# Kernel tuning notes

Measured on AMD Instinct MI355X. Metric: run time of the kernel, lower is better.

The kernel has to match this reference:

```python
import jax, jax.numpy as jnp
import numpy as np

CAPACITY_FACTOR = 1.0  # fairseq Top1Gate default


def setup_inputs() -> dict:
    key = jax.random.key(0)
    ks = jax.random.split(key, 5)
    B, T, M, H, O, E = 8, 1024, 1024, 4096, 1024, 4
    return {
        "hidden_states": jax.random.normal(ks[0], (B, T, M), jnp.float32),
        "gate_w": jax.random.normal(ks[1], (M, E), jnp.float32) * 0.02,
        "fc1_w": jax.random.normal(ks[2], (E, M, H), jnp.float32) * 0.02,
        "fc1_b": jnp.zeros((E, H), jnp.float32),
        "fc2_w": jax.random.normal(ks[3], (E, H, O), jnp.float32) * 0.02,
        "fc2_b": jnp.zeros((E, O), jnp.float32),
    }


def reference(hidden_states, gate_w, fc1_w, fc1_b, fc2_w, fc2_b):
    B, T, M = hidden_states.shape
    E = gate_w.shape[1]
    S = B * T
    C = int(CAPACITY_FACTOR * -(-S // E))  # ceil(S/E)

    features = hidden_states.reshape(S, M)  # [S, M]

    # ---- Top1 gate (fairseq top1gating, eval path: no shuffle/noise) ----
    logits = features @ gate_w                      # [S, E]
    gates = jax.nn.softmax(logits, axis=1)          # [S, E]
    idx = jnp.argmax(gates, axis=1)                 # [S]
    mask1 = jax.nn.one_hot(idx, E, dtype=gates.dtype)  # [S, E]

    # load-balancing aux loss (computed before capacity dropping)
    me = jnp.mean(gates, axis=0)
    ce = jnp.mean(mask1, axis=0)
    l_aux = jnp.sum(me * ce) * E

    # capacity: position within each expert's queue; drop overflow tokens
    locations = jnp.cumsum(mask1, axis=0) - 1.0     # [S, E]
    mask1 = mask1 * (locations < C)
    loc_s = jnp.sum(locations * mask1, axis=1).astype(jnp.int32)  # [S]
    gates1_s = jnp.sum(gates * mask1, axis=1)       # [S] gate value (0 if dropped)

    # combine_weights [S, E, C] and boolean dispatch mask (as float for mm)
    combine = (gates1_s[:, None, None] * mask1[:, :, None]
               * jax.nn.one_hot(loc_s, C, dtype=gates.dtype)[:, None, :])
    dispatch = (combine > 0).astype(features.dtype)  # [S, E, C]

    # ---- dispatch via dense one-hot matmul: [E*C, S] @ [S, M] ----
    dispatch_ecs = jnp.transpose(dispatch, (1, 2, 0)).reshape(E * C, S)
    dispatched = (dispatch_ecs @ features).reshape(E, C, M)

    # ---- per-expert MLP (grouped GEMM) ----
    h = jax.nn.gelu(jnp.einsum('ecm,emh->ech', dispatched, fc1_w) + fc1_b[:, None, :])
    expert_out = jnp.einsum('ech,eho->eco', h, fc2_w) + fc2_b[:, None, :]  # [E, C, O]

    # ---- combine via dense matmul: [S, E*C] @ [E*C, O] ----
    O = expert_out.shape[-1]
    combined = combine.reshape(S, E * C) @ expert_out.reshape(E * C, O)

    return combined.reshape(B, T, O), l_aux
```

## Files before the change

kernel.cpp:

```cpp
#include <hip/hip_runtime.h>
#include <stdint.h>

#define S_TOK 8192
#define MDIM  1024
#define HDIM  4096
#define ODIM  1024
#define NEXP  4
#define CAP   2048

typedef __attribute__((ext_vector_type(8))) short short8;
typedef __attribute__((ext_vector_type(4))) float floatx4;

__device__ __forceinline__ unsigned short f2bf(float x) {
  union { float f; unsigned u; } v; v.f = x;
  unsigned r = v.u + 0x7FFFu + ((v.u >> 16) & 1u);
  return (unsigned short)(r >> 16);
}

__device__ __forceinline__ void gl_lds16(const void* g, void* l) {
  __builtin_amdgcn_global_load_lds(
      (const __attribute__((address_space(1))) void*)g,
      (__attribute__((address_space(3))) void*)l, 16, 0, 0);
}

__device__ __forceinline__ float gelu_tanh(float x) {
  float z = 0.7978845608028654f * (x + 0.044715f * x * x * x);
  float t = 1.0f - 2.0f / (__expf(2.0f * z) + 1.0f);
  return 0.5f * x * (1.0f + t);
}

__global__ __launch_bounds__(256) void gate_kernel(
    const float* __restrict__ feat, const float* __restrict__ gw,
    int* __restrict__ idx, float* __restrict__ gval, float* __restrict__ gsum)
{
  int wave = threadIdx.x >> 6, lane = threadIdx.x & 63;
  int s = blockIdx.x * 4 + wave;
  const float* f = feat + (size_t)s * MDIM;
  double a0 = 0, a1 = 0, a2 = 0, a3 = 0;
  #pragma unroll
  for (int j = 0; j < 16; ++j) {
    int m = lane + j * 64;
    float x = f[m];
    float4 w = ((const float4*)gw)[m];
    a0 += (double)x * w.x; a1 += (double)x * w.y;
    a2 += (double)x * w.z; a3 += (double)x * w.w;
  }
  #pragma unroll
  for (int off = 32; off; off >>= 1) {
    a0 += __shfl_down(a0, off); a1 += __shfl_down(a1, off);
    a2 += __shfl_down(a2, off); a3 += __shfl_down(a3, off);
  }
  __shared__ float bs[4];
  if (threadIdx.x < 4) bs[threadIdx.x] = 0.f;
  __syncthreads();
  if (lane == 0) {
    double lg[4] = {a0, a1, a2, a3};
    double mx = lg[0]; int bi = 0;
    #pragma unroll
    for (int e = 1; e < 4; ++e) if (lg[e] > mx) { mx = lg[e]; bi = e; }
    float ex[4]; float den = 0.f;
    #pragma unroll
    for (int e = 0; e < 4; ++e) { ex[e] = __expf((float)(lg[e] - mx)); den += ex[e]; }
    float inv = 1.f / den;
    idx[s]  = bi;
    gval[s] = ex[bi] * inv;
    #pragma unroll
    for (int e = 0; e < 4; ++e) atomicAdd(&bs[e], ex[e] * inv);
  }
  __syncthreads();
  if (threadIdx.x < 4) atomicAdd(&gsum[threadIdx.x], bs[threadIdx.x]);
}

__global__ __launch_bounds__(1024) void scan_kernel(
    const int* __restrict__ idx, int* __restrict__ perm,
    int* __restrict__ ne, const float* __restrict__ gsum,
    float* __restrict__ laux)
{
  const int tid = threadIdx.x, wave = tid >> 6, lane = tid & 63;
  __shared__ int cnt[16][4];
  __shared__ int off[16][4];
  __shared__ int tot[4];
  unsigned long long below = (lane == 0) ? 0ull : ((~0ull) >> (64 - lane));

  int myE[8], loc[8];
  int c[4] = {0, 0, 0, 0};
  #pragma unroll
  for (int j = 0; j < 8; ++j) {
    int s = wave * 512 + j * 64 + lane;
    int ev = idx[s];
    myE[j] = ev;
    #pragma unroll
    for (int e = 0; e < 4; ++e) {
      unsigned long long mb = __ballot(ev == e);
      if (ev == e) loc[j] = c[e] + __popcll(mb & below);
      c[e] += __popcll(mb);
    }
  }
  if (lane == 0) {
    #pragma unroll
    for (int e = 0; e < 4; ++e) cnt[wave][e] = c[e];
  }
  __syncthreads();
  if (tid < 64) {
    int w = tid >> 2, e = tid & 3;
    int o = 0;
    for (int w2 = 0; w2 < 16; ++w2) if (w2 < w) o += cnt[w2][e];
    off[w][e] = o;
    if (w == 15) tot[e] = o + cnt[15][e];
  }
  __syncthreads();
  #pragma unroll
  for (int j = 0; j < 8; ++j) {
    int s = wave * 512 + j * 64 + lane;
    int e = myE[j];
    int rank = off[wave][e] + loc[j];
    if (rank < CAP) perm[e * CAP + rank] = s;
  }
  if (tid < 4) ne[tid] = tot[tid] < CAP ? tot[tid] : CAP;
  if (tid == 0) {
    float l = 0.f;
    #pragma unroll
    for (int e = 0; e < 4; ++e)
      l += (gsum[e] * (1.0f / S_TOK)) * ((float)tot[e] * (1.0f / S_TOK));
    *laux = l * (float)NEXP;
  }
}

__global__ __launch_bounds__(256) void transpose_cast(
    const float* __restrict__ in, unsigned short* __restrict__ out, int R, int Cc)
{
  __shared__ unsigned short tile[64][66];
  in  += (size_t)blockIdx.z * R * Cc;
  out += (size_t)blockIdx.z * R * Cc;
  int c0 = blockIdx.x * 64, r0 = blockIdx.y * 64;
  int tx = threadIdx.x & 15;
  int ty = threadIdx.x >> 4;
  #pragma unroll
  for (int p = 0; p < 4; ++p) {
    int r = ty + p * 16;
    float4 v = *(const float4*)(in + (size_t)(r0 + r) * Cc + c0 + tx * 4);
    tile[r][tx * 4 + 0] = f2bf(v.x);
    tile[r][tx * 4 + 1] = f2bf(v.y);
    tile[r][tx * 4 + 2] = f2bf(v.z);
    tile[r][tx * 4 + 3] = f2bf(v.w);
  }
  __syncthreads();
  #pragma unroll
  for (int p = 0; p < 4; ++p) {
    int c = ty + p * 16;
    ushort4 o;
    o.x = tile[tx * 4 + 0][c];
    o.y = tile[tx * 4 + 1][c];
    o.z = tile[tx * 4 + 2][c];
    o.w = tile[tx * 4 + 3][c];
    *(ushort4*)(out + (size_t)(c0 + c) * R + r0 + tx * 4) = o;
  }
}

__global__ __launch_bounds__(256) void gather_kernel(
    const float* __restrict__ feat, const int* __restrict__ perm,
    const int* __restrict__ ne, unsigned short* __restrict__ disp)
{
  int b = blockIdx.x;
  int e = b >> 11, c = b & (CAP - 1);
  int m = threadIdx.x * 4;
  ushort4 o;
  if (c < ne[e]) {
    int s = perm[b];
    float4 v = *(const float4*)(feat + (size_t)s * MDIM + m);
    o.x = f2bf(v.x); o.y = f2bf(v.y); o.z = f2bf(v.z); o.w = f2bf(v.w);
  } else {
    o.x = o.y = o.z = o.w = 0;
  }
  *(ushort4*)(disp + (size_t)b * MDIM + m) = o;
}

__global__ __launch_bounds__(256) void fc1_kernel(
    const unsigned short* __restrict__ A, const unsigned short* __restrict__ Bt,
    const float* __restrict__ b1, unsigned short* __restrict__ Hb)
{
  const int e = blockIdx.z, nb = blockIdx.x, mb = blockIdx.y;
  const int tid = threadIdx.x, wave = tid >> 6, lane = tid & 63;

  __shared__ __align__(16) unsigned short smA[128 * 32];
  __shared__ __align__(16) unsigned short smB[128 * 32];

  const char* Ag = (const char*)(A + ((size_t)e * CAP + (size_t)mb * 128) * MDIM);
  const char* Bg = (const char*)(Bt + ((size_t)e * HDIM + (size_t)nb * 128) * MDIM);

  int boff0 = (wave * 2 + 0) * 1024 + lane * 16;
  int boff1 = (wave * 2 + 1) * 1024 + lane * 16;
  const char* agp0 = Ag + (size_t)(boff0 >> 6) * 2048 + (boff0 & 63);
  const char* agp1 = Ag + (size_t)(boff1 >> 6) * 2048 + (boff1 & 63);
  const char* bgp0 = Bg + (size_t)(boff0 >> 6) * 2048 + (boff0 & 63);
  const char* bgp1 = Bg + (size_t)(boff1 >> 6) * 2048 + (boff1 & 63);
  unsigned short* sA0 = smA + (wave * 2 + 0) * 512;
  unsigned short* sA1 = smA + (wave * 2 + 1) * 512;
  unsigned short* sB0 = smB + (wave * 2 + 0) * 512;
  unsigned short* sB1 = smB + (wave * 2 + 1) * 512;

  const int wm = (wave & 1) * 64, wn = (wave >> 1) * 64;
  const int fr = lane & 15, fq = lane >> 4;

  floatx4 acc[4][4] = {};

  for (int kt = 0; kt < MDIM / 32; ++kt) {
    int kb = kt * 64;
    gl_lds16(agp0 + kb, sA0);
    gl_lds16(agp1 + kb, sA1);
    gl_lds16(bgp0 + kb, sB0);
    gl_lds16(bgp1 + kb, sB1);
    __syncthreads();
    short8 af[4], bfr[4];
    #pragma unroll
    for (int i = 0; i < 4; ++i)
      af[i] = *(const short8*)&smA[(wm + i * 16 + fr) * 32 + fq * 8];
    #pragma unroll
    for (int j = 0; j < 4; ++j)
      bfr[j] = *(const short8*)&smB[(wn + j * 16 + fr) * 32 + fq * 8];
    #pragma unroll
    for (int i = 0; i < 4; ++i)
      #pragma unroll
      for (int j = 0; j < 4; ++j)
        acc[i][j] = __builtin_amdgcn_mfma_f32_16x16x32_bf16(af[i], bfr[j], acc[i][j], 0, 0, 0);
    __syncthreads();
  }

  unsigned short* Hrow = Hb + (size_t)e * CAP * HDIM;
  #pragma unroll
  for (int j = 0; j < 4; ++j) {
    int gn = nb * 128 + wn + j * 16 + fr;
    float bv = b1[e * HDIM + gn];
    #pragma unroll
    for (int i = 0; i < 4; ++i) {
      int m0 = mb * 128 + wm + i * 16 + fq * 4;
      #pragma unroll
      for (int r = 0; r < 4; ++r)
        Hrow[(size_t)(m0 + r) * HDIM + gn] = f2bf(gelu_tanh(acc[i][j][r] + bv));
    }
  }
}

__global__ __launch_bounds__(256) void fc2_kernel(
    const unsigned short* __restrict__ A, const unsigned short* __restrict__ Bt,
    const float* __restrict__ b2, const int* __restrict__ perm,
    const int* __restrict__ ne, const float* __restrict__ gval,
    float* __restrict__ out)
{
  const int e = blockIdx.z, nb = blockIdx.x, mb = blockIdx.y;
  const int tid = threadIdx.x, wave = tid >> 6, lane = tid & 63;

  __shared__ __align__(16) unsigned short smA[64 * 32];
  __shared__ __align__(16) unsigned short smB[128 * 32];

  const char* Ag = (const char*)(A + ((size_t)e * CAP + (size_t)mb * 64) * HDIM);
  const char* Bg = (const char*)(Bt + ((size_t)e * ODIM + (size_t)nb * 128) * HDIM);

  int boffA = tid * 16;
  const char* agp = Ag + (size_t)(boffA >> 6) * 8192 + (boffA & 63);
  unsigned short* sA = smA + wave * 512;
  int boff0 = (wave * 2 + 0) * 1024 + lane * 16;
  int boff1 = (wave * 2 + 1) * 1024 + lane * 16;
  const char* bgp0 = Bg + (size_t)(boff0 >> 6) * 8192 + (boff0 & 63);
  const char* bgp1 = Bg + (size_t)(boff1 >> 6) * 8192 + (boff1 & 63);
  unsigned short* sB0 = smB + (wave * 2 + 0) * 512;
  unsigned short* sB1 = smB + (wave * 2 + 1) * 512;

  const int wm = (wave & 1) * 32, wn = (wave >> 1) * 64;
  const int fr = lane & 15, fq = lane >> 4;

  floatx4 acc[2][4] = {};

  for (int kt = 0; kt < HDIM / 32; ++kt) {
    int kb = kt * 64;
    gl_lds16(agp + kb, sA);
    gl_lds16(bgp0 + kb, sB0);
    gl_lds16(bgp1 + kb, sB1);
    __syncthreads();
    short8 af[2], bfr[4];
    #pragma unroll
    for (int i = 0; i < 2; ++i)
      af[i] = *(const short8*)&smA[(wm + i * 16 + fr) * 32 + fq * 8];
    #pragma unroll
    for (int j = 0; j < 4; ++j)
      bfr[j] = *(const short8*)&smB[(wn + j * 16 + fr) * 32 + fq * 8];
    #pragma unroll
    for (int i = 0; i < 2; ++i)
      #pragma unroll
      for (int j = 0; j < 4; ++j)
        acc[i][j] = __builtin_amdgcn_mfma_f32_16x16x32_bf16(af[i], bfr[j], acc[i][j], 0, 0, 0);
    __syncthreads();
  }

  const int nE = ne[e];
  float b2v[4];
  #pragma unroll
  for (int j = 0; j < 4; ++j)
    b2v[j] = b2[e * ODIM + nb * 128 + wn + j * 16 + fr];
  #pragma unroll
  for (int i = 0; i < 2; ++i) {
    #pragma unroll
    for (int r = 0; r < 4; ++r) {
      int c = mb * 64 + wm + i * 16 + fq * 4 + r;
      if (c < nE) {
        int s = perm[e * CAP + c];
        float g = gval[s];
        float* orow = out + (size_t)s * ODIM + nb * 128 + wn;
        #pragma unroll
        for (int j = 0; j < 4; ++j)
          orow[j * 16 + fr] = (acc[i][j][r] + b2v[j]) * g;
      }
    }
  }
}

extern "C" void kernel_launch(void* const* d_in, const int* in_sizes, int n_in,
                              void* d_out, int out_size, void* d_ws, size_t ws_size,
                              hipStream_t stream) {
  const float* feat = (const float*)d_in[0];
  const float* gw   = (const float*)d_in[1];
  const float* w1   = (const float*)d_in[2];
  const float* b1   = (const float*)d_in[3];
  const float* w2   = (const float*)d_in[4];
  const float* b2   = (const float*)d_in[5];
  float* out = (float*)d_out;

  char* ws = (char*)d_ws;
  unsigned short* wt   = (unsigned short*)(ws);
  unsigned short* hbuf = (unsigned short*)(ws + 33554432);
  unsigned short* disp = (unsigned short*)(ws + 100663296);
  int*   idx  = (int*)  (ws + 117440512);
  float* gval = (float*)(ws + 117473280);
  int*   perm = (int*)  (ws + 117506048);
  float* gsum = (float*)(ws + 117538816);
  int*   ne   = (int*)  (ws + 117538832);

  hipMemsetAsync(d_out, 0, (size_t)S_TOK * ODIM * sizeof(float), stream);
  hipMemsetAsync(ws + 117538816, 0, 32, stream);

  gate_kernel<<<S_TOK / 4, 256, 0, stream>>>(feat, gw, idx, gval, gsum);
  scan_kernel<<<1, 1024, 0, stream>>>(idx, perm, ne, gsum, out + (size_t)S_TOK * ODIM);
  transpose_cast<<<dim3(HDIM / 64, MDIM / 64, NEXP), 256, 0, stream>>>(w1, wt, MDIM, HDIM);
  gather_kernel<<<NEXP * CAP, 256, 0, stream>>>(feat, perm, ne, disp);
  fc1_kernel<<<dim3(HDIM / 128, CAP / 128, NEXP), 256, 0, stream>>>(disp, wt, b1, hbuf);
  transpose_cast<<<dim3(ODIM / 64, HDIM / 64, NEXP), 256, 0, stream>>>(w2, wt, HDIM, ODIM);
  fc2_kernel<<<dim3(ODIM / 128, CAP / 64, NEXP), 256, 0, stream>>>(hbuf, wt, b2, perm, ne, gval, out);
}
```

Baseline: 443.8 us.

## Triple-buffer fc2 LDS loads and remap grid for XCD locality

```diff
diff --git a/kernel.cpp b/kernel.cpp
--- a/kernel.cpp
+++ b/kernel.cpp
@@ -247,49 +247,74 @@
     const int* __restrict__ ne, const float* __restrict__ gval,
     float* __restrict__ out)
 {
-  const int e = blockIdx.z, nb = blockIdx.x, mb = blockIdx.y;
+  const int b = blockIdx.x;
+  const int wg = (b & 7) * 128 + (b >> 3);
+  const int nb = wg & 7, mb = (wg >> 3) & 31, e = wg >> 8;
   const int tid = threadIdx.x, wave = tid >> 6, lane = tid & 63;
 
-  __shared__ __align__(16) unsigned short smA[64 * 32];
-  __shared__ __align__(16) unsigned short smB[128 * 32];
+  __shared__ __align__(16) unsigned short smA[3 * 64 * 32];
+  __shared__ __align__(16) unsigned short smB[3 * 128 * 32];
 
   const char* Ag = (const char*)(A + ((size_t)e * CAP + (size_t)mb * 64) * HDIM);
   const char* Bg = (const char*)(Bt + ((size_t)e * ODIM + (size_t)nb * 128) * HDIM);
 
   int boffA = tid * 16;
   const char* agp = Ag + (size_t)(boffA >> 6) * 8192 + (boffA & 63);
-  unsigned short* sA = smA + wave * 512;
   int boff0 = (wave * 2 + 0) * 1024 + lane * 16;
   int boff1 = (wave * 2 + 1) * 1024 + lane * 16;
   const char* bgp0 = Bg + (size_t)(boff0 >> 6) * 8192 + (boff0 & 63);
   const char* bgp1 = Bg + (size_t)(boff1 >> 6) * 8192 + (boff1 & 63);
-  unsigned short* sB0 = smB + (wave * 2 + 0) * 512;
-  unsigned short* sB1 = smB + (wave * 2 + 1) * 512;
+
+  const int ldsA_w = wave * 512;
+  const int ldsB_w0 = (wave * 2 + 0) * 512;
+  const int ldsB_w1 = (wave * 2 + 1) * 512;
 
   const int wm = (wave & 1) * 32, wn = (wave >> 1) * 64;
   const int fr = lane & 15, fq = lane >> 4;
 
   floatx4 acc[2][4] = {};
 
-  for (int kt = 0; kt < HDIM / 32; ++kt) {
-    int kb = kt * 64;
-    gl_lds16(agp + kb, sA);
-    gl_lds16(bgp0 + kb, sB0);
-    gl_lds16(bgp1 + kb, sB1);
-    __syncthreads();
+  const int NT = HDIM / 32;
+  int c0 = 0, c1 = 1, c2 = 2;
+
+  {
+    gl_lds16(agp + 0 * 64,  smA + 0 * 2048 + ldsA_w);
+    gl_lds16(bgp0 + 0 * 64, smB + 0 * 4096 + ldsB_w0);
+    gl_lds16(bgp1 + 0 * 64, smB + 0 * 4096 + ldsB_w1);
+    gl_lds16(agp + 1 * 64,  smA + 1 * 2048 + ldsA_w);
+    gl_lds16(bgp0 + 1 * 64, smB + 1 * 4096 + ldsB_w0);
+    gl_lds16(bgp1 + 1 * 64, smB + 1 * 4096 + ldsB_w1);
+  }
+  asm volatile("s_waitcnt vmcnt(3)" ::: "memory");
+  __builtin_amdgcn_s_barrier();
+
+  for (int kt = 0; kt < NT; ++kt) {
+    if (kt + 2 < NT) {
+      int kb = (kt + 2) * 64;
+      gl_lds16(agp + kb,  smA + c2 * 2048 + ldsA_w);
+      gl_lds16(bgp0 + kb, smB + c2 * 4096 + ldsB_w0);
+      gl_lds16(bgp1 + kb, smB + c2 * 4096 + ldsB_w1);
+    }
+    const unsigned short* sA = smA + c0 * 2048;
+    const unsigned short* sB = smB + c0 * 4096;
     short8 af[2], bfr[4];
     #pragma unroll
     for (int i = 0; i < 2; ++i)
-      af[i] = *(const short8*)&smA[(wm + i * 16 + fr) * 32 + fq * 8];
+      af[i] = *(const short8*)&sA[(wm + i * 16 + fr) * 32 + fq * 8];
     #pragma unroll
     for (int j = 0; j < 4; ++j)
-      bfr[j] = *(const short8*)&smB[(wn + j * 16 + fr) * 32 + fq * 8];
+      bfr[j] = *(const short8*)&sB[(wn + j * 16 + fr) * 32 + fq * 8];
     #pragma unroll
     for (int i = 0; i < 2; ++i)
       #pragma unroll
       for (int j = 0; j < 4; ++j)
         acc[i][j] = __builtin_amdgcn_mfma_f32_16x16x32_bf16(af[i], bfr[j], acc[i][j], 0, 0, 0);
-    __syncthreads();
+    if (kt + 1 < NT) {
+      if (kt + 2 < NT) asm volatile("s_waitcnt vmcnt(3)" ::: "memory");
+      else             asm volatile("s_waitcnt vmcnt(0)" ::: "memory");
+      __builtin_amdgcn_s_barrier();
+    }
+    int t = c0; c0 = c1; c1 = c2; c2 = t;
   }
 
   const int nE = ne[e];
@@ -344,5 +369,5 @@
   gather_kernel<<<NEXP * CAP, 256, 0, stream>>>(feat, perm, ne, disp);
   fc1_kernel<<<dim3(HDIM / 128, CAP / 128, NEXP), 256, 0, stream>>>(disp, wt, b1, hbuf);
   transpose_cast<<<dim3(ODIM / 64, HDIM / 64, NEXP), 256, 0, stream>>>(w2, wt, HDIM, ODIM);
-  fc2_kernel<<<dim3(ODIM / 128, CAP / 64, NEXP), 256, 0, stream>>>(hbuf, wt, b2, perm, ne, gval, out);
-}
+  fc2_kernel<<<1024, 256, 0, stream>>>(hbuf, wt, b2, perm, ne, gval, out);
+}
```

New measurement: 431.4 us. -2.8%, faster.
